# Performance work log

Hardware: AMD Instinct MI355X
Metric: run time of the kernel (lower is better)

Reference implementation:

```python
import jax, jax.numpy as jnp
import numpy as np

B, S, IN, N, MOT = 128, 4096, 6, 64, 3
ODE_UNFOLDS = 6
EPS = 1e-8


def setup_inputs() -> dict:
    ks = jax.random.split(jax.random.key(0), 20)
    u = lambda k, shape, lo, hi: jax.random.uniform(k, shape, jnp.float32, lo, hi)
    pm1 = lambda k, shape: jnp.where(jax.random.bernoulli(k, 0.5, shape), 1.0, -1.0).astype(jnp.float32)
    return {
        "x": jax.random.normal(ks[0], (B, S, IN), jnp.float32),
        "mean_us": 0.1 * jax.random.normal(ks[1], (IN,), jnp.float32),
        "std_us": u(ks[2], (IN,), 0.5, 1.5),
        "input_w": u(ks[3], (IN,), 0.8, 1.2),
        "input_b": 0.01 * jax.random.normal(ks[4], (IN,), jnp.float32),
        "output_w": u(ks[5], (MOT,), 0.8, 1.2),
        "output_b": 0.01 * jax.random.normal(ks[6], (MOT,), jnp.float32),
        "gleak": u(ks[7], (N,), 0.001, 1.0),
        "vleak": u(ks[8], (N,), -0.2, 0.2),
        "cm": u(ks[9], (N,), 0.4, 0.6),
        "sensory_W": u(ks[10], (IN, N), 0.001, 1.0),
        "sensory_mu": u(ks[11], (IN, N), 0.3, 0.8),
        "sensory_sigma": u(ks[12], (IN, N), 3.0, 8.0),
        "sensory_erev": pm1(ks[13], (IN, N)),
        "W": u(ks[14], (N, N), 0.001, 1.0),
        "mu": u(ks[15], (N, N), 0.3, 0.8),
        "sigma": u(ks[16], (N, N), 3.0, 8.0),
        "erev": pm1(ks[17], (N, N)),
    }


def _ltc_sequence(x, mean_us, std_us, input_w, input_b, output_w, output_b,
                  gleak, vleak, cm, sensory_W, sensory_mu, sensory_sigma,
                  sensory_erev, W, mu, sigma, erev):
    # normalize inputs (DgaRawSequence) then LTCCell input mapping
    xn = (x - mean_us) / std_us                      # [B,S,IN]
    xm = xn * input_w + input_b                      # [B,S,IN]
    cm_t = cm * ODE_UNFOLDS                          # cm / (elapsed_time=1 / ode_unfolds)

    def step(v, u_t):                                # v: [B,N], u_t: [B,IN]
        # sensory synapse activations [B,IN,N]
        s_act = sensory_W * jax.nn.sigmoid((u_t[:, :, None] - sensory_mu) * sensory_sigma)
        wns = jnp.sum(s_act * sensory_erev, axis=1)  # [B,N]
        wds = jnp.sum(s_act, axis=1)                 # [B,N]
        for _ in range(ODE_UNFOLDS):
            w_act = W * jax.nn.sigmoid((v[:, :, None] - mu) * sigma)  # [B,N,N]
            num = cm_t * v + gleak * vleak + jnp.sum(w_act * erev, axis=1) + wns
            den = cm_t + gleak + jnp.sum(w_act, axis=1) + wds
            v = num / (den + EPS)
        return v, v

    v0 = jnp.zeros((x.shape[0], gleak.shape[0]), dtype=x.dtype)
    _, vs = jax.lax.scan(step, v0, jnp.swapaxes(xm, 0, 1))   # [S,B,N]
    states = jnp.swapaxes(vs, 0, 1)                          # [B,S,N]
    # LTCCell output mapping (motor neurons = first MOT states)
    out = states[..., :MOT] * output_w + output_b            # [B,S,3]
    # denormalize (DgaRawSequence)
    return out * std_us[:MOT] + mean_us[:MOT]


def reference(x, mean_us, std_us, input_w, input_b, output_w, output_b,
              gleak, vleak, cm, sensory_W, sensory_mu, sensory_sigma,
              sensory_erev, W, mu, sigma, erev):
    return _ltc_sequence(x, mean_us, std_us, input_w, input_b, output_w,
                         output_b, gleak, vleak, cm, sensory_W, sensory_mu,
                         sensory_sigma, sensory_erev, W, mu, sigma, erev)
```

## Files before the change

### kernel.cpp

```cpp
#include <hip/hip_runtime.h>

#define B_ 128
#define S_ 4096
#define IN_ 6
#define N_ 64
#define MOT_ 3
#define UNF 6
#define EPS_ 1e-8f
#define LOG2E 1.4426950408889634f

__device__ __forceinline__ float red16(float x) {
#if __has_builtin(__builtin_amdgcn_permlane16_swap)
    auto r = __builtin_amdgcn_permlane16_swap(__float_as_int(x), __float_as_int(x),
                                              false, false);
    return __int_as_float((int)r[0]) + __int_as_float((int)r[1]);
#else
    return x + __shfl_xor(x, 16, 64);
#endif
}
__device__ __forceinline__ float red32(float x) {
#if __has_builtin(__builtin_amdgcn_permlane32_swap)
    auto r = __builtin_amdgcn_permlane32_swap(__float_as_int(x), __float_as_int(x),
                                              false, false);
    return __int_as_float((int)r[0]) + __int_as_float((int)r[1]);
#else
    return x + __shfl_xor(x, 32, 64);
#endif
}

__device__ __forceinline__ void lds_barrier() {
    asm volatile("s_waitcnt lgkmcnt(0)" ::: "memory");
    __builtin_amdgcn_s_barrier();
}

__launch_bounds__(256, 1)
__global__ void ltc_kernel(
    const float* __restrict__ x,
    const float* __restrict__ mean_us, const float* __restrict__ std_us,
    const float* __restrict__ input_w, const float* __restrict__ input_b,
    const float* __restrict__ output_w, const float* __restrict__ output_b,
    const float* __restrict__ gleak, const float* __restrict__ vleak,
    const float* __restrict__ cm,
    const float* __restrict__ sW, const float* __restrict__ sMu,
    const float* __restrict__ sSig, const float* __restrict__ sErev,
    const float* __restrict__ W, const float* __restrict__ Mu,
    const float* __restrict__ Sig, const float* __restrict__ Erev,
    float* __restrict__ out)
{
    const int b    = blockIdx.x;
    const int t    = threadIdx.x;
    const int lane = t & 63;
    const int w    = t >> 6;
    const int cc   = lane >> 4;
    const int ii   = lane & 15;
    const int myCol = w * 16 + ii;
    const int jb   = cc * 16;

    __shared__ __align__(16) float vbuf[2][N_];
    __shared__ float s_lds[IN_][N_][2];

    float A[16], Bc[16], Wr[16], We[16];
#pragma unroll
    for (int jj = 0; jj < 16; ++jj) {
        int idx = (jb + jj) * N_ + myCol;
        float sg = Sig[idx], m = Mu[idx], ww = W[idx], e = Erev[idx];
        A[jj]  = -sg * LOG2E;
        Bc[jj] = m * sg * LOG2E;
        Wr[jj] = ww;
        We[jj] = ww * e;
    }

    const float cmt = cm[myCol] * (float)UNF;
    const float glk = gleak[myCol];
    const float gv  = glk * vleak[myCol];
    const float dbase = cmt + glk + EPS_;

    const int i0 = w;
    const int i1 = w + 4;
    const bool has1 = (w < 2);
    float SA0, SB0, SWv0, SWe0, ns0, nb0;
    {
        int idx = i0 * N_ + lane;
        float sg = sSig[idx], m = sMu[idx], ww = sW[idx], e = sErev[idx];
        SA0 = -sg * LOG2E; SB0 = m * sg * LOG2E; SWv0 = ww; SWe0 = ww * e;
        ns0 = input_w[i0] / std_us[i0];
        nb0 = input_b[i0] - mean_us[i0] / std_us[i0] * input_w[i0];
    }
    float SA1 = 0.f, SB1 = 0.f, SWv1 = 0.f, SWe1 = 0.f, ns1 = 0.f, nb1 = 0.f;
    if (has1) {
        int idx = i1 * N_ + lane;
        float sg = sSig[idx], m = sMu[idx], ww = sW[idx], e = sErev[idx];
        SA1 = -sg * LOG2E; SB1 = m * sg * LOG2E; SWv1 = ww; SWe1 = ww * e;
        ns1 = input_w[i1] / std_us[i1];
        nb1 = input_b[i1] - mean_us[i1] / std_us[i1] * input_w[i1];
    }

    float OW = 0.f, OB = 0.f;
    if (t < MOT_) {
        OW = output_w[t] * std_us[t];
        OB = output_b[t] * std_us[t] + mean_us[t];
    }

    const float* xb = x + (size_t)b * S_ * IN_;
    float* ob = out + (size_t)b * S_ * MOT_;

    if (t < N_) vbuf[0][t] = 0.f;
    {
        float u  = fmaf(xb[i0], ns0, nb0);
        float e  = __builtin_amdgcn_exp2f(fmaf(u, SA0, SB0));
        float sg = __builtin_amdgcn_rcpf(1.0f + e);
        s_lds[i0][lane][0] = SWe0 * sg;
        s_lds[i0][lane][1] = SWv0 * sg;
        if (has1) {
            float u1  = fmaf(xb[i1], ns1, nb1);
            float e1  = __builtin_amdgcn_exp2f(fmaf(u1, SA1, SB1));
            float sg1 = __builtin_amdgcn_rcpf(1.0f + e1);
            s_lds[i1][lane][0] = SWe1 * sg1;
            s_lds[i1][lane][1] = SWv1 * sg1;
        }
    }
    lds_barrier();

    float v_my = 0.f;

    for (int s = 0; s < S_; ++s) {
        const int s1 = (s + 1 < S_) ? (s + 1) : s;
        int off0 = s1 * IN_ + i0;
        asm volatile("" : "+v"(off0));
        float xn0 = xb[off0];
        float xn1 = 0.f;
        if (has1) {
            int off1 = s1 * IN_ + i1;
            asm volatile("" : "+v"(off1));
            xn1 = xb[off1];
        }

        float a = 0.f, d = 0.f;
#pragma unroll
        for (int ci = 0; ci < IN_; ++ci) {
            float2 sv = *(const float2*)&s_lds[ci][myCol][0];
            a += sv.x; d += sv.y;
        }
        const float nb = gv + a;
        const float db = dbase + d;

#pragma unroll
        for (int k = 0; k < UNF; ++k) {
            const int p = k & 1;
            float4 v0 = *(const float4*)&vbuf[p][jb];
            float4 v1 = *(const float4*)&vbuf[p][jb + 4];
            float4 v2 = *(const float4*)&vbuf[p][jb + 8];
            float4 v3 = *(const float4*)&vbuf[p][jb + 12];
            const float vj[16] = {v0.x, v0.y, v0.z, v0.w, v1.x, v1.y, v1.z, v1.w,
                                  v2.x, v2.y, v2.z, v2.w, v3.x, v3.y, v3.z, v3.w};

            float pn = 0.f, pd = 0.f;
#pragma unroll
            for (int q = 0; q < 4; ++q) {
                const int j0 = q * 4;
                float t0 = 1.0f + __builtin_amdgcn_exp2f(fmaf(vj[j0+0], A[j0+0], Bc[j0+0]));
                float t1 = 1.0f + __builtin_amdgcn_exp2f(fmaf(vj[j0+1], A[j0+1], Bc[j0+1]));
                float t2 = 1.0f + __builtin_amdgcn_exp2f(fmaf(vj[j0+2], A[j0+2], Bc[j0+2]));
                float t3 = 1.0f + __builtin_amdgcn_exp2f(fmaf(vj[j0+3], A[j0+3], Bc[j0+3]));
                float p01 = t0 * t1, p23 = t2 * t3;
                float r   = __builtin_amdgcn_rcpf(p01 * p23);
                float ne01 = fmaf(We[j0+0], t1, We[j0+1] * t0);
                float ne23 = fmaf(We[j0+2], t3, We[j0+3] * t2);
                float nr01 = fmaf(Wr[j0+0], t1, Wr[j0+1] * t0);
                float nr23 = fmaf(Wr[j0+2], t3, Wr[j0+3] * t2);
                float NE = fmaf(ne01, p23, ne23 * p01);
                float NR = fmaf(nr01, p23, nr23 * p01);
                pn = fmaf(NE, r, pn);
                pd = fmaf(NR, r, pd);
            }

            pn = red16(pn);  pd = red16(pd);
            pn = red32(pn);  pd = red32(pd);

            float num = fmaf(cmt, v_my, nb + pn);
            v_my = num * __builtin_amdgcn_rcpf(db + pd);

            if (cc == 0) vbuf[p ^ 1][myCol] = v_my;

            if (k == 1) {
                float u  = fmaf(xn0, ns0, nb0);
                float e2 = __builtin_amdgcn_exp2f(fmaf(u, SA0, SB0));
                float sg = __builtin_amdgcn_rcpf(1.0f + e2);
                s_lds[i0][lane][0] = SWe0 * sg;
                s_lds[i0][lane][1] = SWv0 * sg;
                if (has1) {
                    float u1  = fmaf(xn1, ns1, nb1);
                    float e3  = __builtin_amdgcn_exp2f(fmaf(u1, SA1, SB1));
                    float sg1 = __builtin_amdgcn_rcpf(1.0f + e3);
                    s_lds[i1][lane][0] = SWe1 * sg1;
                    s_lds[i1][lane][1] = SWv1 * sg1;
                }
            }
            lds_barrier();
        }

        if (t < MOT_) ob[s * MOT_ + t] = fmaf(v_my, OW, OB);
    }
}

extern "C" void kernel_launch(void* const* d_in, const int* in_sizes, int n_in,
                              void* d_out, int out_size, void* d_ws, size_t ws_size,
                              hipStream_t stream) {
    (void)in_sizes; (void)n_in; (void)d_ws; (void)ws_size; (void)out_size;
    const float* x       = (const float*)d_in[0];
    const float* mean_us = (const float*)d_in[1];
    const float* std_us  = (const float*)d_in[2];
    const float* input_w = (const float*)d_in[3];
    const float* input_b = (const float*)d_in[4];
    const float* out_w   = (const float*)d_in[5];
    const float* out_b   = (const float*)d_in[6];
    const float* gleak   = (const float*)d_in[7];
    const float* vleak   = (const float*)d_in[8];
    const float* cm      = (const float*)d_in[9];
    const float* sW      = (const float*)d_in[10];
    const float* sMu     = (const float*)d_in[11];
    const float* sSig    = (const float*)d_in[12];
    const float* sErev   = (const float*)d_in[13];
    const float* W       = (const float*)d_in[14];
    const float* Mu      = (const float*)d_in[15];
    const float* Sig     = (const float*)d_in[16];
    const float* Erev    = (const float*)d_in[17];
    float* out = (float*)d_out;

    ltc_kernel<<<dim3(B_), dim3(256), 0, stream>>>(
        x, mean_us, std_us, input_w, input_b, out_w, out_b,
        gleak, vleak, cm, sW, sMu, sSig, sErev, W, Mu, Sig, Erev, out);
}
```

Measured before the change: 10.16 ms.

## Replace workgroup barriers with per-wave LDS flag spin-waits and double-buffer sensory LDS

```diff
diff --git a/kernel.cpp b/kernel.cpp
--- a/kernel.cpp
+++ b/kernel.cpp
@@ -26,11 +26,6 @@
 #else
     return x + __shfl_xor(x, 32, 64);
 #endif
-}
-
-__device__ __forceinline__ void lds_barrier() {
-    asm volatile("s_waitcnt lgkmcnt(0)" ::: "memory");
-    __builtin_amdgcn_s_barrier();
 }
 
 __launch_bounds__(256, 1)
@@ -54,20 +49,25 @@
     const int cc   = lane >> 4;
     const int ii   = lane & 15;
     const int myCol = w * 16 + ii;
-    const int jb   = cc * 16;
+    const int cc4  = cc * 4;
 
     __shared__ __align__(16) float vbuf[2][N_];
-    __shared__ float s_lds[IN_][N_][2];
+    __shared__ int vflag[2][4];
+    __shared__ float s_lds[2][IN_][N_][2];
 
     float A[16], Bc[16], Wr[16], We[16];
 #pragma unroll
-    for (int jj = 0; jj < 16; ++jj) {
-        int idx = (jb + jj) * N_ + myCol;
-        float sg = Sig[idx], m = Mu[idx], ww = W[idx], e = Erev[idx];
-        A[jj]  = -sg * LOG2E;
-        Bc[jj] = m * sg * LOG2E;
-        Wr[jj] = ww;
-        We[jj] = ww * e;
+    for (int q = 0; q < 4; ++q) {
+#pragma unroll
+        for (int r = 0; r < 4; ++r) {
+            int j   = q * 16 + cc4 + r;
+            int idx = j * N_ + myCol;
+            float sg = Sig[idx], m = Mu[idx], ww = W[idx], e = Erev[idx];
+            A[q*4+r]  = -sg * LOG2E;
+            Bc[q*4+r] = m * sg * LOG2E;
+            Wr[q*4+r] = ww;
+            We[q*4+r] = ww * e;
+        }
     }
 
     const float cmt = cm[myCol] * (float)UNF;
@@ -105,23 +105,25 @@
     float* ob = out + (size_t)b * S_ * MOT_;
 
     if (t < N_) vbuf[0][t] = 0.f;
+    if (t < 8)  vflag[t >> 2][t & 3] = 0;
     {
         float u  = fmaf(xb[i0], ns0, nb0);
         float e  = __builtin_amdgcn_exp2f(fmaf(u, SA0, SB0));
         float sg = __builtin_amdgcn_rcpf(1.0f + e);
-        s_lds[i0][lane][0] = SWe0 * sg;
-        s_lds[i0][lane][1] = SWv0 * sg;
+        s_lds[0][i0][lane][0] = SWe0 * sg;
+        s_lds[0][i0][lane][1] = SWv0 * sg;
         if (has1) {
             float u1  = fmaf(xb[i1], ns1, nb1);
             float e1  = __builtin_amdgcn_exp2f(fmaf(u1, SA1, SB1));
             float sg1 = __builtin_amdgcn_rcpf(1.0f + e1);
-            s_lds[i1][lane][0] = SWe1 * sg1;
-            s_lds[i1][lane][1] = SWv1 * sg1;
-        }
-    }
-    lds_barrier();
+            s_lds[0][i1][lane][0] = SWe1 * sg1;
+            s_lds[0][i1][lane][1] = SWv1 * sg1;
+        }
+    }
+    __syncthreads();
 
     float v_my = 0.f;
+    int mbase = 0;
 
     for (int s = 0; s < S_; ++s) {
         const int s1 = (s + 1 < S_) ? (s + 1) : s;
@@ -135,69 +137,79 @@
             xn1 = xb[off1];
         }
 
+        const int sp = s & 1;
         float a = 0.f, d = 0.f;
 #pragma unroll
         for (int ci = 0; ci < IN_; ++ci) {
-            float2 sv = *(const float2*)&s_lds[ci][myCol][0];
+            float2 sv = *(const float2*)&s_lds[sp][ci][myCol][0];
             a += sv.x; d += sv.y;
         }
-        const float nb = gv + a;
-        const float db = dbase + d;
+        const float nbs = gv + a;
+        const float dbs = dbase + d;
 
 #pragma unroll
         for (int k = 0; k < UNF; ++k) {
-            const int p = k & 1;
-            float4 v0 = *(const float4*)&vbuf[p][jb];
-            float4 v1 = *(const float4*)&vbuf[p][jb + 4];
-            float4 v2 = *(const float4*)&vbuf[p][jb + 8];
-            float4 v3 = *(const float4*)&vbuf[p][jb + 12];
-            const float vj[16] = {v0.x, v0.y, v0.z, v0.w, v1.x, v1.y, v1.z, v1.w,
-                                  v2.x, v2.y, v2.z, v2.w, v3.x, v3.y, v3.z, v3.w};
-
-            float pn = 0.f, pd = 0.f;
+            const int par  = k & 1;
+            const int need = mbase + k;
+
+            for (;;) {
+                int f0 = __hip_atomic_load(&vflag[par][0], __ATOMIC_RELAXED, __HIP_MEMORY_SCOPE_WORKGROUP);
+                int f1 = __hip_atomic_load(&vflag[par][1], __ATOMIC_RELAXED, __HIP_MEMORY_SCOPE_WORKGROUP);
+                int f2 = __hip_atomic_load(&vflag[par][2], __ATOMIC_RELAXED, __HIP_MEMORY_SCOPE_WORKGROUP);
+                int f3 = __hip_atomic_load(&vflag[par][3], __ATOMIC_RELAXED, __HIP_MEMORY_SCOPE_WORKGROUP);
+                if (f0 >= need && f1 >= need && f2 >= need && f3 >= need) break;
+            }
+            asm volatile("" ::: "memory");
+
+            float pnq[4], pdq[4];
 #pragma unroll
             for (int q = 0; q < 4; ++q) {
-                const int j0 = q * 4;
-                float t0 = 1.0f + __builtin_amdgcn_exp2f(fmaf(vj[j0+0], A[j0+0], Bc[j0+0]));
-                float t1 = 1.0f + __builtin_amdgcn_exp2f(fmaf(vj[j0+1], A[j0+1], Bc[j0+1]));
-                float t2 = 1.0f + __builtin_amdgcn_exp2f(fmaf(vj[j0+2], A[j0+2], Bc[j0+2]));
-                float t3 = 1.0f + __builtin_amdgcn_exp2f(fmaf(vj[j0+3], A[j0+3], Bc[j0+3]));
-                float p01 = t0 * t1, p23 = t2 * t3;
-                float r   = __builtin_amdgcn_rcpf(p01 * p23);
-                float ne01 = fmaf(We[j0+0], t1, We[j0+1] * t0);
-                float ne23 = fmaf(We[j0+2], t3, We[j0+3] * t2);
-                float nr01 = fmaf(Wr[j0+0], t1, Wr[j0+1] * t0);
-                float nr23 = fmaf(Wr[j0+2], t3, Wr[j0+3] * t2);
-                float NE = fmaf(ne01, p23, ne23 * p01);
-                float NR = fmaf(nr01, p23, nr23 * p01);
-                pn = fmaf(NE, r, pn);
-                pd = fmaf(NR, r, pd);
+                float4 cv = *(const float4*)&vbuf[par][q * 16 + cc4];
+                float c0 = cv.x, c1 = cv.y, c2 = cv.z, c3 = cv.w;
+                float e0 = __builtin_amdgcn_exp2f(fmaf(c0, A[q*4+0], Bc[q*4+0]));
+                float e1 = __builtin_amdgcn_exp2f(fmaf(c1, A[q*4+1], Bc[q*4+1]));
+                float e2 = __builtin_amdgcn_exp2f(fmaf(c2, A[q*4+2], Bc[q*4+2]));
+                float e3 = __builtin_amdgcn_exp2f(fmaf(c3, A[q*4+3], Bc[q*4+3]));
+                float s0 = __builtin_amdgcn_rcpf(1.0f + e0);
+                float s1x = __builtin_amdgcn_rcpf(1.0f + e1);
+                float s2 = __builtin_amdgcn_rcpf(1.0f + e2);
+                float s3 = __builtin_amdgcn_rcpf(1.0f + e3);
+                pnq[q] = fmaf(We[q*4+0], s0, fmaf(We[q*4+1], s1x,
+                         fmaf(We[q*4+2], s2, We[q*4+3] * s3)));
+                pdq[q] = fmaf(Wr[q*4+0], s0, fmaf(Wr[q*4+1], s1x,
+                         fmaf(Wr[q*4+2], s2, Wr[q*4+3] * s3)));
             }
+            float pn = (pnq[0] + pnq[1]) + (pnq[2] + pnq[3]);
+            float pd = (pdq[0] + pdq[1]) + (pdq[2] + pdq[3]);
 
             pn = red16(pn);  pd = red16(pd);
             pn = red32(pn);  pd = red32(pd);
 
-            float num = fmaf(cmt, v_my, nb + pn);
-            v_my = num * __builtin_amdgcn_rcpf(db + pd);
-
-            if (cc == 0) vbuf[p ^ 1][myCol] = v_my;
+            v_my = fmaf(cmt, v_my, nbs + pn) * __builtin_amdgcn_rcpf(dbs + pd);
+
+            if (lane < 16) vbuf[par ^ 1][w * 16 + lane] = v_my;
 
             if (k == 1) {
                 float u  = fmaf(xn0, ns0, nb0);
-                float e2 = __builtin_amdgcn_exp2f(fmaf(u, SA0, SB0));
-                float sg = __builtin_amdgcn_rcpf(1.0f + e2);
-                s_lds[i0][lane][0] = SWe0 * sg;
-                s_lds[i0][lane][1] = SWv0 * sg;
+                float e4 = __builtin_amdgcn_exp2f(fmaf(u, SA0, SB0));
+                float sg = __builtin_amdgcn_rcpf(1.0f + e4);
+                s_lds[sp ^ 1][i0][lane][0] = SWe0 * sg;
+                s_lds[sp ^ 1][i0][lane][1] = SWv0 * sg;
                 if (has1) {
                     float u1  = fmaf(xn1, ns1, nb1);
-                    float e3  = __builtin_amdgcn_exp2f(fmaf(u1, SA1, SB1));
-                    float sg1 = __builtin_amdgcn_rcpf(1.0f + e3);
-                    s_lds[i1][lane][0] = SWe1 * sg1;
-                    s_lds[i1][lane][1] = SWv1 * sg1;
+                    float e5  = __builtin_amdgcn_exp2f(fmaf(u1, SA1, SB1));
+                    float sg1 = __builtin_amdgcn_rcpf(1.0f + e5);
+                    s_lds[sp ^ 1][i1][lane][0] = SWe1 * sg1;
+                    s_lds[sp ^ 1][i1][lane][1] = SWv1 * sg1;
                 }
             }
-            lds_barrier();
-        }
+
+            asm volatile("s_waitcnt lgkmcnt(0)" ::: "memory");
+            if (lane == 0)
+                __hip_atomic_store(&vflag[par ^ 1][w], need + 1,
+                                   __ATOMIC_RELAXED, __HIP_MEMORY_SCOPE_WORKGROUP);
+        }
+        mbase += UNF;
 
         if (t < MOT_) ob[s * MOT_ + t] = fmaf(v_my, OW, OB);
     }
```

New measurement: 12.11 ms. 1.19x slower.
